# Optimization experiments

Measured on AMD Instinct MI355X. Metric: run time of the kernel, lower is better.

Reference implementation:

```python
import jax, jax.numpy as jnp
import numpy as np

N_MEMBERS = 2      # ensemble_length=3, loop runs i=1..2
N_NODES = 65536    # batch_size * total_length = 32 * 2048
N_EDGES = 1_048_576
N_LAYERS = 12      # num_conv_layers
D = 64             # constant feature width (linspace 64->64)


def setup_inputs() -> dict:
    key = jax.random.key(0)
    k0, k1, k2, k3 = jax.random.split(key, 4)
    x = jax.random.normal(k0, (N_MEMBERS, N_NODES, D), dtype=jnp.float32)
    edge_index = jax.random.randint(k1, (N_MEMBERS, 2, N_EDGES), 0, N_NODES, dtype=jnp.int64)
    # GCNConv weights per member/layer; scale ~ 1/sqrt(D) for stability across 12 layers
    W = jax.random.normal(k2, (N_MEMBERS, N_LAYERS, D, D), dtype=jnp.float32) / jnp.sqrt(jnp.float32(D))
    b = jax.random.normal(k3, (N_MEMBERS, N_LAYERS, D), dtype=jnp.float32) * 0.01
    return {"x": x, "edge_index": edge_index, "W": W, "b": b}


def gcn_conv(h, src, dst, W, b):
    """PyG GCNConv: add self-loops, symmetric D^-1/2 (A+I) D^-1/2 normalization,
    linear transform, bias."""
    hw = h @ W                                                # [N, D_out]
    # degree includes the self-loop (+1)
    deg = jax.ops.segment_sum(jnp.ones((src.shape[0],), h.dtype), dst,
                              num_segments=N_NODES) + jnp.asarray(1.0, h.dtype)
    dinv = jax.lax.rsqrt(deg)                                 # [N]
    norm = dinv[src] * dinv[dst]                              # [E]
    agg = jax.ops.segment_sum(norm[:, None] * hw[src], dst, num_segments=N_NODES)
    agg = agg + (dinv * dinv)[:, None] * hw                   # self-loop term
    return agg + b


def reference(x, edge_index, W, b):
    # eval mode: F.dropout(training=False) is identity
    outs = []
    for i in range(N_MEMBERS):
        src, dst = edge_index[i, 0], edge_index[i, 1]
        h = x[i]
        for j in range(N_LAYERS - 1):
            h = jax.nn.relu(gcn_conv(h, src, dst, W[i, j], b[i, j]))
        outs.append(gcn_conv(h, src, dst, W[i, N_LAYERS - 1], b[i, N_LAYERS - 1]))
    return jnp.stack(outs)  # [N_MEMBERS, N_NODES, D]
```

## Files before the change

kernel.cpp:

```cpp
#include <hip/hip_runtime.h>
#include <hip/hip_fp16.h>
#include <math.h>

#define N_MEMBERS 2
#define N_NODES   65536
#define N_EDGES   1048576
#define N_LAYERS  12
#define D         64
#define OFF_STRIDE (N_NODES + 1)
#define NODE_MASK (N_NODES - 1)

#define NBINS       256
#define BIN_CAP     5120
#define EDGES_PER_WG 4096

typedef _Float16 f16;
typedef f16   f16x8 __attribute__((ext_vector_type(8)));
typedef float f32x4 __attribute__((ext_vector_type(4)));


__global__ __launch_bounds__(256) void bin_scatter_k(const int* __restrict__ ei,
                                                     int* __restrict__ binCursor,
                                                     unsigned int* __restrict__ binned) {
    int m = blockIdx.y;
    int t = threadIdx.x;
    int eBase = blockIdx.x * EDGES_PER_WG;
    __shared__ int hist[NBINS];
    __shared__ int base[NBINS];
    hist[t] = 0;
    __syncthreads();
    const int* srcp = ei + (size_t)(m * 2 + 0) * N_EDGES;
    const int* dstp = ei + (size_t)(m * 2 + 1) * N_EDGES;
    unsigned int pk[16];
    int bn[16], rk[16];
    #pragma unroll
    for (int i = 0; i < 16; i++) {
        int e = eBase + i * 256 + t;
        int src = srcp[e] & NODE_MASK;
        int dst = dstp[e] & NODE_MASK;
        int b = dst >> 8;
        bn[i] = b;
        pk[i] = ((unsigned)src << 8) | (unsigned)(dst & 255);
        rk[i] = atomicAdd(&hist[b], 1);
    }
    __syncthreads();
    base[t] = atomicAdd(&binCursor[m * NBINS + t], hist[t]);
    __syncthreads();
    unsigned int* bb = binned + (size_t)m * NBINS * BIN_CAP;
    #pragma unroll
    for (int i = 0; i < 16; i++) {
        int pos = base[bn[i]] + rk[i];
        if (pos < BIN_CAP)
            bb[(size_t)bn[i] * BIN_CAP + pos] = pk[i];
    }
}

__global__ __launch_bounds__(256) void scan_bins_k(const int* __restrict__ cur,
                                                   int* __restrict__ bbase) {
    int m = blockIdx.x, t = threadIdx.x;
    __shared__ int sh[256];
    int v0 = cur[m * NBINS + t];
    sh[t] = v0;
    __syncthreads();
    for (int ofs = 1; ofs < 256; ofs <<= 1) {
        int v = sh[t];
        int a = (t >= ofs) ? sh[t - ofs] : 0;
        __syncthreads();
        sh[t] = v + a;
        __syncthreads();
    }
    bbase[m * NBINS + t] = sh[t] - v0;
}

__global__ __launch_bounds__(256) void bin_build_k(const unsigned int* __restrict__ binned,
                                                   const int* __restrict__ binCursor,
                                                   const int* __restrict__ bbase,
                                                   int* __restrict__ off,
                                                   float* __restrict__ dinv,
                                                   unsigned short* __restrict__ csr_src) {
    int m = blockIdx.y, b = blockIdx.x, t = threadIdx.x;
    int cnt   = binCursor[m * NBINS + b];
    int gbase = bbase[m * NBINS + b];
    const unsigned int* bb = binned + ((size_t)m * NBINS + b) * BIN_CAP;
    __shared__ int degl[256];
    __shared__ int offl[256];
    degl[t] = 0;
    __syncthreads();
    unsigned int ed[20];
    #pragma unroll
    for (int j = 0; j < 20; j++) {
        int i = t + j * 256;
        ed[j] = 0;
        if (i < cnt) {
            unsigned int w = bb[i];
            int r = atomicAdd(&degl[w & 255], 1);
            ed[j] = w | ((unsigned)r << 24);
        }
    }
    __syncthreads();
    int myDeg = degl[t];
    offl[t] = myDeg;
    __syncthreads();
    for (int ofs = 1; ofs < 256; ofs <<= 1) {
        int v = offl[t];
        int a = (t >= ofs) ? offl[t - ofs] : 0;
        __syncthreads();
        offl[t] = v + a;
        __syncthreads();
    }
    int myOff = gbase + offl[t] - myDeg;
    int node = b * 256 + t;
    off[m * OFF_STRIDE + node] = myOff;
    if (b == NBINS - 1 && t == 255) off[m * OFF_STRIDE + N_NODES] = N_EDGES;
    dinv[m * N_NODES + node] = 1.0f / sqrtf((float)myDeg + 1.0f);
    offl[t] = myOff;
    __syncthreads();
    unsigned short* cs = csr_src + (size_t)m * N_EDGES;
    #pragma unroll
    for (int j = 0; j < 20; j++) {
        int i = t + j * 256;
        if (i < cnt) {
            int dl  = ed[j] & 255;
            int src = (ed[j] >> 8) & 0xFFFF;
            int r   = ed[j] >> 24;
            cs[offl[dl] + r] = (unsigned short)src;
        }
    }
}

__global__ __launch_bounds__(256) void prescale_k(const float* __restrict__ x,
                                                  const float* __restrict__ dinv,
                                                  __half* __restrict__ g) {
    int i = blockIdx.x * 256 + threadIdx.x;
    float dv = dinv[i >> 3];
    float4 a = ((const float4*)x)[i * 2];
    float4 b = ((const float4*)x)[i * 2 + 1];
    union { __half2 h2[4]; uint4 u; } p;
    p.h2[0] = __floats2half2_rn(dv * a.x, dv * a.y);
    p.h2[1] = __floats2half2_rn(dv * a.z, dv * a.w);
    p.h2[2] = __floats2half2_rn(dv * b.x, dv * b.y);
    p.h2[3] = __floats2half2_rn(dv * b.z, dv * b.w);
    ((uint4*)g)[i] = p.u;
}

__device__ __forceinline__ void cvt8(uint4 u, float* f) {
    const __half2* h2 = (const __half2*)&u;
    #pragma unroll
    for (int i = 0; i < 4; i++) {
        float2 t = __half22float2(h2[i]);
        f[2 * i]     = t.x;
        f[2 * i + 1] = t.y;
    }
}

__global__ __launch_bounds__(256) void aggregate_k(const __half* __restrict__ g,
                                                   __half* __restrict__ S,
                                                   const int* __restrict__ off,
                                                   const unsigned short* __restrict__ csr_src,
                                                   const float* __restrict__ dinv) {
    int bflat = blockIdx.x;
    int xcd   = bflat & 7;
    int m     = xcd >> 2;
    int slot  = ((bflat >> 3) << 2) | (xcd & 3);
    int n = slot * 4 + (threadIdx.x >> 6);
    int lane = threadIdx.x & 63;
    int fg   = lane & 7;
    int sub  = lane >> 3;
    const __half*         gm = g + (size_t)m * N_NODES * D;
    const int*            ob = off + m * OFF_STRIDE;
    const unsigned short* sb = csr_src + (size_t)m * N_EDGES;

    float acc[8];
    #pragma unroll
    for (int i = 0; i < 8; i++) acc[i] = 0.f;

    int e0 = ob[n], e1 = ob[n + 1];
    #pragma unroll 2
    for (int e = e0; e < e1; e += 8) {
        int ee  = e + sub;
        int idx = (ee < e1) ? ee : (e1 - 1);
        int s   = sb[idx];
        float w = (ee < e1) ? 1.0f : 0.0f;
        uint4 gv = *(const uint4*)(gm + (size_t)s * D + fg * 8);
        float f[8];
        cvt8(gv, f);
        #pragma unroll
        for (int i = 0; i < 8; i++) acc[i] = fmaf(w, f[i], acc[i]);
    }
    #pragma unroll
    for (int msk = 8; msk < 64; msk <<= 1)
        #pragma unroll
        for (int i = 0; i < 8; i++) acc[i] += __shfl_xor(acc[i], msk);

    float dv = dinv[m * N_NODES + n];
    uint4 sg = *(const uint4*)(gm + (size_t)n * D + fg * 8);
    float sf[8];
    cvt8(sg, sf);
    if (sub == 0) {
        union { __half2 h2[4]; uint4 u; } p;
        #pragma unroll
        for (int i = 0; i < 4; i++)
            p.h2[i] = __floats2half2_rn(dv * (acc[2 * i]     + sf[2 * i]),
                                        dv * (acc[2 * i + 1] + sf[2 * i + 1]));
        *(uint4*)(S + (size_t)m * N_NODES * D + (size_t)n * D + fg * 8) = p.u;
    }
}

__global__ __launch_bounds__(256) void gemm_f16_k(const __half* __restrict__ S,
                                                  const float* __restrict__ Wall,
                                                  const float* __restrict__ dinv,
                                                  const float* __restrict__ ball,
                                                  __half* __restrict__ gout,
                                                  float* __restrict__ fout,
                                                  int layer, int last) {
    int m = blockIdx.y;
    const float* Wg = Wall + (size_t)(m * N_LAYERS + layer) * D * D;
    __shared__ __align__(16) _Float16 Whi[D][72];
    __shared__ __align__(16) _Float16 Wlo[D][72];
    for (int idx = threadIdx.x; idx < D * D / 4; idx += 256) {
        float4 v = ((const float4*)Wg)[idx];
        int k  = idx >> 4;
        int c0 = (idx & 15) << 2;
        float vv[4] = {v.x, v.y, v.z, v.w};
        #pragma unroll
        for (int i = 0; i < 4; i++) {
            f16 hi = (f16)vv[i];
            Whi[c0 + i][k] = hi;
            Wlo[c0 + i][k] = (f16)(vv[i] - (float)hi);
        }
    }
    __syncthreads();

    int lane = threadIdx.x & 63;
    int wav  = threadIdx.x >> 6;
    int nn   = lane & 15;
    int quad = lane >> 4;

    f16x8 Bh[8], Bl[8];
    #pragma unroll
    for (int t = 0; t < 4; t++)
        #pragma unroll
        for (int s = 0; s < 2; s++) {
            Bh[t * 2 + s] = *(const f16x8*)&Whi[t * 16 + nn][s * 32 + quad * 8];
            Bl[t * 2 + s] = *(const f16x8*)&Wlo[t * 16 + nn][s * 32 + quad * 8];
        }

    const __half* Sm = S + (size_t)m * N_NODES * D;
    const float*  dm = dinv + m * N_NODES;
    const float*  bp = ball + (size_t)(m * N_LAYERS + layer) * D;
    __half*       gm = gout + (size_t)m * N_NODES * D;
    float*        fm = fout + (size_t)m * N_NODES * D;

    float4 b4[4];
    #pragma unroll
    for (int t = 0; t < 4; t++)
        b4[t] = *(const float4*)(bp + t * 16 + quad * 4);

    int base = blockIdx.x * 256 + wav * 64;
    for (int g = 0; g < 4; g++) {
        int node = base + g * 16 + nn;
        const __half* srow = Sm + (size_t)node * D;
        f16x8 a0 = *(const f16x8*)(srow + quad * 8);
        f16x8 a1 = *(const f16x8*)(srow + 32 + quad * 8);
        float dv = dm[node];
        #pragma unroll
        for (int t = 0; t < 4; t++) {
            f32x4 c = {0.f, 0.f, 0.f, 0.f};
            c = __builtin_amdgcn_mfma_f32_16x16x32_f16(Bh[t * 2 + 0], a0, c, 0, 0, 0);
            c = __builtin_amdgcn_mfma_f32_16x16x32_f16(Bh[t * 2 + 1], a1, c, 0, 0, 0);
            c = __builtin_amdgcn_mfma_f32_16x16x32_f16(Bl[t * 2 + 0], a0, c, 0, 0, 0);
            c = __builtin_amdgcn_mfma_f32_16x16x32_f16(Bl[t * 2 + 1], a1, c, 0, 0, 0);
            float v0 = (float)c[0] + b4[t].x;
            float v1 = (float)c[1] + b4[t].y;
            float v2 = (float)c[2] + b4[t].z;
            float v3 = (float)c[3] + b4[t].w;
            int col = t * 16 + quad * 4;
            if (last) {
                *(float4*)(fm + (size_t)node * D + col) = make_float4(v0, v1, v2, v3);
            } else {
                union { __half2 h2[2]; uint2 u; } p;
                p.h2[0] = __floats2half2_rn(fmaxf(v0, 0.f) * dv, fmaxf(v1, 0.f) * dv);
                p.h2[1] = __floats2half2_rn(fmaxf(v2, 0.f) * dv, fmaxf(v3, 0.f) * dv);
                *(uint2*)(gm + (size_t)node * D + col) = p.u;
            }
        }
    }
}


extern "C" void kernel_launch(void* const* d_in, const int* in_sizes, int n_in,
                              void* d_out, int out_size, void* d_ws, size_t ws_size,
                              hipStream_t stream) {
    (void)in_sizes; (void)n_in; (void)out_size; (void)ws_size;
    const float* x  = (const float*)d_in[0];
    const int*   ei = (const int*)d_in[1];
    const float* W  = (const float*)d_in[2];
    const float* b  = (const float*)d_in[3];
    float* out = (float*)d_out;

    char* ws = (char*)d_ws;
    size_t o = 0;
    auto take = [&](size_t bytes) -> void* {
        void* p = ws + o;
        o = (o + bytes + 255) & ~(size_t)255;
        return p;
    };
    float*          dinv      = (float*) take((size_t)N_MEMBERS * N_NODES * 4);
    int*            off       = (int*)   take((size_t)N_MEMBERS * OFF_STRIDE * 4);
    int*            binCursor = (int*)   take((size_t)N_MEMBERS * NBINS * 4);
    int*            bbase     = (int*)   take((size_t)N_MEMBERS * NBINS * 4);
    unsigned short* csr_src   = (unsigned short*)take((size_t)N_MEMBERS * N_EDGES * 2);
    __half*         gbuf      = (__half*)take((size_t)N_MEMBERS * N_NODES * D * 2);
    __half*         Sbuf      = (__half*)take((size_t)N_MEMBERS * N_NODES * D * 2);
    unsigned int*   binned    = (unsigned int*)Sbuf;

    hipMemsetAsync(binCursor, 0, (size_t)N_MEMBERS * NBINS * 4, stream);

    bin_scatter_k<<<dim3(N_EDGES / EDGES_PER_WG, N_MEMBERS), 256, 0, stream>>>(
        ei, binCursor, binned);
    scan_bins_k<<<dim3(N_MEMBERS), 256, 0, stream>>>(binCursor, bbase);
    bin_build_k<<<dim3(NBINS, N_MEMBERS), 256, 0, stream>>>(
        binned, binCursor, bbase, off, dinv, csr_src);
    prescale_k<<<dim3((N_MEMBERS * N_NODES * D / 8) / 256), 256, 0, stream>>>(
        x, dinv, gbuf);

    for (int j = 0; j < N_LAYERS; j++) {
        aggregate_k<<<dim3(N_MEMBERS * (N_NODES / 4)), 256, 0, stream>>>(
            gbuf, Sbuf, off, csr_src, dinv);
        gemm_f16_k<<<dim3(N_NODES / 256, N_MEMBERS), 256, 0, stream>>>(
            Sbuf, W, dinv, b, gbuf, out, j, (j == N_LAYERS - 1) ? 1 : 0);
    }
}
```

Measured before the change: 874.8 us.

## Batch four nodes per wave in aggregation and pre-split weights for GEMM

The aggregation kernel now has each wavefront process four destination nodes at once, interleaving their gathers to expose more memory-level parallelism. It also launches a quarter as many blocks. Weights are split into fp16 hi/lo once, up front, in MFMA fragment order, so the GEMM kernel loads fragments directly instead of rebuilding them in LDS every layer. The GEMM kernel also halves nodes per block to double its grid. The cost is that a wave's loop length follows the highest-degree node of its four, wasting lanes when degrees differ, and register use rises.

```diff
diff --git a/kernel.cpp b/kernel.cpp
--- a/kernel.cpp
+++ b/kernel.cpp
@@ -128,6 +128,32 @@
     }
 }
 
+__global__ __launch_bounds__(256) void presplit_k(const float* __restrict__ Wall,
+                                                  __half* __restrict__ Wsplit) {
+    int gid = blockIdx.x * 256 + threadIdx.x;
+    int ml   = gid >> 9;
+    int r    = gid & 511;
+    int t    = (r >> 7) & 3;
+    int s    = (r >> 6) & 1;
+    int lane = r & 63;
+    int c  = t * 16 + (lane & 15);
+    int k0 = s * 32 + (lane >> 4) * 8;
+    const float* Wg = Wall + (size_t)ml * D * D;
+    __half* base = Wsplit + (size_t)ml * 8192;
+    int fo = ((t * 2 + s) * 64 + lane) * 8;
+    __half hi8[8], lo8[8];
+    #pragma unroll
+    for (int j = 0; j < 8; j++) {
+        float v = Wg[(k0 + j) * D + c];
+        f16 h = (f16)v;
+        hi8[j] = *(__half*)&h;
+        f16 l = (f16)(v - (float)h);
+        lo8[j] = *(__half*)&l;
+    }
+    *(uint4*)(base + fo)        = *(uint4*)hi8;
+    *(uint4*)(base + 4096 + fo) = *(uint4*)lo8;
+}
+
 __global__ __launch_bounds__(256) void prescale_k(const float* __restrict__ x,
                                                   const float* __restrict__ dinv,
                                                   __half* __restrict__ g) {
@@ -162,7 +188,8 @@
     int xcd   = bflat & 7;
     int m     = xcd >> 2;
     int slot  = ((bflat >> 3) << 2) | (xcd & 3);
-    int n = slot * 4 + (threadIdx.x >> 6);
+    int wav   = threadIdx.x >> 6;
+    int n0    = slot * 16 + wav * 4;
     int lane = threadIdx.x & 63;
     int fg   = lane & 7;
     int sub  = lane >> 3;
@@ -170,79 +197,84 @@
     const int*            ob = off + m * OFF_STRIDE;
     const unsigned short* sb = csr_src + (size_t)m * N_EDGES;
 
-    float acc[8];
-    #pragma unroll
-    for (int i = 0; i < 8; i++) acc[i] = 0.f;
-
-    int e0 = ob[n], e1 = ob[n + 1];
+    float acc[4][8];
+    #pragma unroll
+    for (int j = 0; j < 4; j++)
+        #pragma unroll
+        for (int i = 0; i < 8; i++) acc[j][i] = 0.f;
+
+    int o[5];
+    #pragma unroll
+    for (int j = 0; j < 5; j++) o[j] = ob[n0 + j];
+    int dm01 = max(o[1] - o[0], o[2] - o[1]);
+    int dm23 = max(o[3] - o[2], o[4] - o[3]);
+    int iters = (max(dm01, dm23) + 7) >> 3;
+
     #pragma unroll 2
-    for (int e = e0; e < e1; e += 8) {
-        int ee  = e + sub;
-        int idx = (ee < e1) ? ee : (e1 - 1);
-        int s   = sb[idx];
-        float w = (ee < e1) ? 1.0f : 0.0f;
-        uint4 gv = *(const uint4*)(gm + (size_t)s * D + fg * 8);
-        float f[8];
-        cvt8(gv, f);
-        #pragma unroll
-        for (int i = 0; i < 8; i++) acc[i] = fmaf(w, f[i], acc[i]);
+    for (int it = 0; it < iters; it++) {
+        int ofs = it * 8 + sub;
+        #pragma unroll
+        for (int j = 0; j < 4; j++) {
+            int ia  = o[j] + ofs;
+            int lim = o[j + 1];
+            int idx = (ia < lim) ? ia : (lim - 1);
+            float w = (ia < lim) ? 1.0f : 0.0f;
+            int s   = sb[idx];
+            uint4 gv = *(const uint4*)(gm + (size_t)s * D + fg * 8);
+            float f[8];
+            cvt8(gv, f);
+            #pragma unroll
+            for (int i = 0; i < 8; i++) acc[j][i] = fmaf(w, f[i], acc[j][i]);
+        }
     }
     #pragma unroll
     for (int msk = 8; msk < 64; msk <<= 1)
         #pragma unroll
-        for (int i = 0; i < 8; i++) acc[i] += __shfl_xor(acc[i], msk);
-
-    float dv = dinv[m * N_NODES + n];
-    uint4 sg = *(const uint4*)(gm + (size_t)n * D + fg * 8);
-    float sf[8];
-    cvt8(sg, sf);
-    if (sub == 0) {
-        union { __half2 h2[4]; uint4 u; } p;
-        #pragma unroll
-        for (int i = 0; i < 4; i++)
-            p.h2[i] = __floats2half2_rn(dv * (acc[2 * i]     + sf[2 * i]),
-                                        dv * (acc[2 * i + 1] + sf[2 * i + 1]));
-        *(uint4*)(S + (size_t)m * N_NODES * D + (size_t)n * D + fg * 8) = p.u;
+        for (int j = 0; j < 4; j++)
+            #pragma unroll
+            for (int i = 0; i < 8; i++) acc[j][i] += __shfl_xor(acc[j][i], msk);
+
+    __half* Sm = S + (size_t)m * N_NODES * D;
+    #pragma unroll
+    for (int j = 0; j < 4; j++) {
+        if (sub == j) {
+            int n = n0 + j;
+            float dv = dinv[m * N_NODES + n];
+            uint4 sg = *(const uint4*)(gm + (size_t)n * D + fg * 8);
+            float sf[8];
+            cvt8(sg, sf);
+            union { __half2 h2[4]; uint4 u; } p;
+            #pragma unroll
+            for (int i = 0; i < 4; i++)
+                p.h2[i] = __floats2half2_rn(dv * (acc[j][2 * i]     + sf[2 * i]),
+                                            dv * (acc[j][2 * i + 1] + sf[2 * i + 1]));
+            *(uint4*)(Sm + (size_t)n * D + fg * 8) = p.u;
+        }
     }
 }
 
 __global__ __launch_bounds__(256) void gemm_f16_k(const __half* __restrict__ S,
-                                                  const float* __restrict__ Wall,
+                                                  const __half* __restrict__ Wsplit,
                                                   const float* __restrict__ dinv,
                                                   const float* __restrict__ ball,
                                                   __half* __restrict__ gout,
                                                   float* __restrict__ fout,
                                                   int layer, int last) {
     int m = blockIdx.y;
-    const float* Wg = Wall + (size_t)(m * N_LAYERS + layer) * D * D;
-    __shared__ __align__(16) _Float16 Whi[D][72];
-    __shared__ __align__(16) _Float16 Wlo[D][72];
-    for (int idx = threadIdx.x; idx < D * D / 4; idx += 256) {
-        float4 v = ((const float4*)Wg)[idx];
-        int k  = idx >> 4;
-        int c0 = (idx & 15) << 2;
-        float vv[4] = {v.x, v.y, v.z, v.w};
-        #pragma unroll
-        for (int i = 0; i < 4; i++) {
-            f16 hi = (f16)vv[i];
-            Whi[c0 + i][k] = hi;
-            Wlo[c0 + i][k] = (f16)(vv[i] - (float)hi);
-        }
-    }
-    __syncthreads();
-
     int lane = threadIdx.x & 63;
     int wav  = threadIdx.x >> 6;
     int nn   = lane & 15;
     int quad = lane >> 4;
 
+    const __half* Wf = Wsplit + (size_t)(m * N_LAYERS + layer) * 8192;
     f16x8 Bh[8], Bl[8];
     #pragma unroll
     for (int t = 0; t < 4; t++)
         #pragma unroll
         for (int s = 0; s < 2; s++) {
-            Bh[t * 2 + s] = *(const f16x8*)&Whi[t * 16 + nn][s * 32 + quad * 8];
-            Bl[t * 2 + s] = *(const f16x8*)&Wlo[t * 16 + nn][s * 32 + quad * 8];
+            int fo = ((t * 2 + s) * 64 + lane) * 8;
+            Bh[t * 2 + s] = *(const f16x8*)(Wf + fo);
+            Bl[t * 2 + s] = *(const f16x8*)(Wf + 4096 + fo);
         }
 
     const __half* Sm = S + (size_t)m * N_NODES * D;
@@ -256,8 +288,9 @@
     for (int t = 0; t < 4; t++)
         b4[t] = *(const float4*)(bp + t * 16 + quad * 4);
 
-    int base = blockIdx.x * 256 + wav * 64;
-    for (int g = 0; g < 4; g++) {
+    int base = blockIdx.x * 128 + wav * 32;
+    #pragma unroll
+    for (int g = 0; g < 2; g++) {
         int node = base + g * 16 + nn;
         const __half* srow = Sm + (size_t)node * D;
         f16x8 a0 = *(const f16x8*)(srow + quad * 8);
@@ -310,12 +343,14 @@
     int*            binCursor = (int*)   take((size_t)N_MEMBERS * NBINS * 4);
     int*            bbase     = (int*)   take((size_t)N_MEMBERS * NBINS * 4);
     unsigned short* csr_src   = (unsigned short*)take((size_t)N_MEMBERS * N_EDGES * 2);
+    __half*         Wsplit    = (__half*)take((size_t)N_MEMBERS * N_LAYERS * 8192 * 2);
     __half*         gbuf      = (__half*)take((size_t)N_MEMBERS * N_NODES * D * 2);
     __half*         Sbuf      = (__half*)take((size_t)N_MEMBERS * N_NODES * D * 2);
     unsigned int*   binned    = (unsigned int*)Sbuf;
 
     hipMemsetAsync(binCursor, 0, (size_t)N_MEMBERS * NBINS * 4, stream);
 
+    presplit_k<<<dim3(N_MEMBERS * N_LAYERS * 512 / 256), 256, 0, stream>>>(W, Wsplit);
     bin_scatter_k<<<dim3(N_EDGES / EDGES_PER_WG, N_MEMBERS), 256, 0, stream>>>(
         ei, binCursor, binned);
     scan_bins_k<<<dim3(N_MEMBERS), 256, 0, stream>>>(binCursor, bbase);
@@ -325,9 +360,9 @@
         x, dinv, gbuf);
 
     for (int j = 0; j < N_LAYERS; j++) {
-        aggregate_k<<<dim3(N_MEMBERS * (N_NODES / 4)), 256, 0, stream>>>(
+        aggregate_k<<<dim3(N_MEMBERS * (N_NODES / 16)), 256, 0, stream>>>(
             gbuf, Sbuf, off, csr_src, dinv);
-        gemm_f16_k<<<dim3(N_NODES / 256, N_MEMBERS), 256, 0, stream>>>(
-            Sbuf, W, dinv, b, gbuf, out, j, (j == N_LAYERS - 1) ? 1 : 0);
-    }
-}
+        gemm_f16_k<<<dim3(N_NODES / 128, N_MEMBERS), 256, 0, stream>>>(
+            Sbuf, Wsplit, dinv, b, gbuf, out, j, (j == N_LAYERS - 1) ? 1 : 0);
+    }
+}
```

Result: faster. 819.1 us (-6.4%).
